# Kernel tuning notes

Measured on AMD Instinct MI355X. Metric: run time of the kernel, lower is better.

## Reference

```python
import jax, jax.numpy as jnp
import numpy as np


def _gcn(x, ei, W, b):
    """PyG-style GCNConv: add self-loops, symmetric deg^-1/2 normalization,
    linear transform, scatter-sum aggregation at target nodes, then bias."""
    n = x.shape[0]
    loops = jnp.arange(n)
    src = jnp.concatenate([ei[0], loops])  # message sources
    dst = jnp.concatenate([ei[1], loops])  # aggregation targets
    deg = jax.ops.segment_sum(jnp.ones(src.shape[0], x.dtype), dst, num_segments=n)
    dinv = jnp.where(deg > 0, jax.lax.rsqrt(deg), jnp.zeros_like(deg))
    h = x @ W  # [N, H]
    norm = (dinv[src] * dinv[dst])[:, None]
    out = jax.ops.segment_sum(h[src] * norm, dst, num_segments=n)
    return out + b


def setup_inputs() -> dict:
    N, E, C, H, O, HOPS = 50000, 1600000, 256, 256, 40, 3
    key = jax.random.key(0)
    ks = jax.random.split(key, 12)

    def xav(k, shp):
        # xavier_uniform with relu gain, as in init_weights
        fan_in, fan_out = shp[-2], shp[-1]
        lim = float(np.sqrt(2.0) * np.sqrt(6.0 / (fan_in + fan_out)))
        return jax.random.uniform(k, shp, jnp.float32, -lim, lim)

    return {
        "x": jax.random.normal(ks[0], (N, C), jnp.float32),
        "edge_index": jax.random.randint(ks[1], (2, E), 0, N),
        "new_edge_indexs": jax.random.randint(ks[2], (HOPS, 2, E), 0, N),
        "W_mlp": xav(ks[3], (C, H)),
        "b_mlp": jnp.zeros((H,), jnp.float32),
        "We1": xav(ks[4], (C, H)),
        "be1": jnp.zeros((H,), jnp.float32),
        "We2": xav(ks[5], (H, H)),
        "be2": jnp.zeros((H,), jnp.float32),
        "Wh": xav(ks[6], (HOPS, C, H)),
        "bh": jnp.zeros((HOPS, H), jnp.float32),
        "att": jnp.ones((HOPS + 2,), jnp.float32),
        "Wc": xav(ks[7], (H * (HOPS + 2), O)),
        "bc": jnp.zeros((O,), jnp.float32),
    }


def reference(x, edge_index, new_edge_indexs, W_mlp, b_mlp, We1, be1, We2, be2,
              Wh, bh, att, Wc, bc):
    hops = Wh.shape[0]
    mask = jax.nn.softmax(att)  # softmax over branch attention weights

    mlp = jax.nn.relu(x @ W_mlp + b_mlp) * mask[0]

    e = jax.nn.relu(_gcn(x, edge_index, We1, be1))
    # dropout(p=0.5) is identity in eval mode
    e = jax.nn.relu(_gcn(e, edge_index, We2, be2)) * mask[1]

    # NOTE: original code uses mask[i+1] per hop (hop 0 shares mask[1] with extra_conv)
    outs = [jax.nn.relu(_gcn(x, new_edge_indexs[i], Wh[i], bh[i])) * mask[i + 1]
            for i in range(hops)]

    z = jnp.concatenate(outs + [e, mlp], axis=1)  # [N, H*(hops+2)]
    z = z @ Wc + bc
    return jax.nn.log_softmax(z, axis=-1)
```

## Files before the change

### kernel.cpp

```cpp
#include <hip/hip_runtime.h>
#include <hip/hip_bf16.h>

typedef unsigned short u16;
typedef unsigned int u32;
typedef unsigned char u8;

typedef __bf16 bf16x8 __attribute__((ext_vector_type(8)));
typedef float f32x4 __attribute__((ext_vector_type(4)));

__device__ __forceinline__ u16 f2b(float f) {
    u32 u = __float_as_uint(f);
    u32 r = u + 0x7fffu + ((u >> 16) & 1u);
    return (u16)(r >> 16);
}
__device__ __forceinline__ u8 f2e4m3(float v) {
    return (u8)(__builtin_amdgcn_cvt_pk_fp8_f32(v, v, 0, false) & 0xff);
}
__device__ __forceinline__ void acc16(float* a, uint4 v) {
    u32 w[4] = {v.x, v.y, v.z, v.w};
#pragma unroll
    for (int q = 0; q < 4; ++q) {
        auto p0 = __builtin_amdgcn_cvt_pk_f32_fp8(w[q], false);
        auto p1 = __builtin_amdgcn_cvt_pk_f32_fp8(w[q], true);
        a[q * 4 + 0] += p0[0]; a[q * 4 + 1] += p0[1];
        a[q * 4 + 2] += p1[0]; a[q * 4 + 3] += p1[1];
    }
}

#define SA 72
#define BSHIFT 8
#define BMAX 256
#define BCAP 12288
#define BINCHUNK 4096
#define GEMM_SMEM (128 * SA * 2 * 2)

__global__ void pack_all(const float* __restrict__ x, u16* __restrict__ x16, int PB, int N,
                         const float* __restrict__ W_mlp, const float* __restrict__ We1,
                         const float* __restrict__ We2, const float* __restrict__ Wh,
                         u16* __restrict__ wt, int HOPS,
                         const float* __restrict__ Wc, u16* __restrict__ wct, int O, int NB, int WCB,
                         const float* __restrict__ att, float* __restrict__ mask,
                         int* __restrict__ bcnt, int SETS) {
    int b = blockIdx.x, t = threadIdx.x;
    if (b < PB) {
        long g = (long)b * 256 + t;
        if (g * 4 < (long)N * 256) {
            float4 v = reinterpret_cast<const float4*>(x)[g];
            ushort4 o; o.x = f2b(v.x); o.y = f2b(v.y); o.z = f2b(v.z); o.w = f2b(v.w);
            reinterpret_cast<ushort4*>(x16)[g] = o;
        }
        return;
    }
    b -= PB;
    int WB = (3 + HOPS) * 256;
    if (b < WB) {
        int y = b >> 8, ib = b & 255;
        const float* W = (y == 0) ? W_mlp : (y == 1) ? We1 : (y == 2) ? We2
                                          : (Wh + (size_t)(y - 3) * 65536);
        int idx = ib * 256 + t;
        int n = idx >> 8, k = idx & 255;
        wt[(size_t)y * 65536 + idx] = f2b(W[k * 256 + n]);
        return;
    }
    b -= WB;
    if (b < WCB) {
        int idx = b * 256 + t;
        if (idx < NB * 48 * 256) {
            int bb = idx / (48 * 256), r = idx - bb * 48 * 256;
            int n = r >> 8, k = r & 255;
            float v = (n < O) ? Wc[((size_t)(bb * 256 + k)) * O + n] : 0.f;
            wct[idx] = f2b(v);
        }
        return;
    }
    for (int i = t; i < SETS * BMAX; i += 256) bcnt[i] = 0;
    if (t == 0) {
        float m = -3.4e38f;
        for (int i = 0; i < NB; ++i) m = fmaxf(m, att[i]);
        float s = 0.f;
        for (int i = 0; i < NB; ++i) { float e = __expf(att[i] - m); mask[i] = e; s += e; }
        for (int i = 0; i < NB; ++i) mask[i] /= s;
    }
}


__global__ __launch_bounds__(256) void bin_edges(
    const int* __restrict__ ei, const int* __restrict__ nei, int E, int B,
    int* __restrict__ bcnt, u32* __restrict__ binned) {
    int set = blockIdx.y;
    const int* src = (set == 0) ? ei : (nei + (size_t)(set - 1) * 2 * E);
    const int* dst = src + E;
    __shared__ u32 ebuf[BINCHUNK];
    __shared__ int hist[BMAX], resv[BMAX], lbase[BMAX], lcur[BMAX], s[BMAX];
    int t = threadIdx.x;
    hist[t] = 0; lcur[t] = 0;
    __syncthreads();
    int base = blockIdx.x * BINCHUNK;
    int lim = min(base + BINCHUNK, E);
    for (int i = base + t; i < lim; i += 256)
        atomicAdd(&hist[dst[i] >> BSHIFT], 1);
    __syncthreads();
    int h = hist[t];
    if (t < B && h > 0) resv[t] = atomicAdd(&bcnt[set * BMAX + t], h);
    s[t] = h;
    __syncthreads();
    for (int off = 1; off < 256; off <<= 1) {
        int x = s[t];
        int add = (t >= off) ? s[t - off] : 0;
        __syncthreads();
        s[t] = x + add;
        __syncthreads();
    }
    lbase[t] = s[t] - h;
    __syncthreads();
    for (int i = base + t; i < lim; i += 256) {
        int d = dst[i];
        int b = d >> BSHIFT;
        int p = atomicAdd(&lcur[b], 1);
        ebuf[lbase[b] + p] = (u32)src[i] | ((u32)d << 16);
    }
    __syncthreads();
    int cnt = lim - base;
    for (int i = t; i < cnt; i += 256) {
        u32 pk = ebuf[i];
        int b = (int)(pk >> (16 + BSHIFT));
        int gpos = resv[b] + (i - lbase[b]);
        if (gpos < BCAP)
            binned[((size_t)set * BMAX + b) * BCAP + gpos] = pk;
    }
}

__global__ void bscan(const int* __restrict__ bcnt, int* __restrict__ bbase,
                      int* __restrict__ rp, int N, int E, int B) {
    int set = blockIdx.x, t = threadIdx.x;
    int v = (t < B) ? bcnt[set * BMAX + t] : 0;
    __shared__ int s[256];
    s[t] = v; __syncthreads();
    for (int off = 1; off < 256; off <<= 1) {
        int x = s[t];
        int add = (t >= off) ? s[t - off] : 0;
        __syncthreads();
        s[t] = x + add;
        __syncthreads();
    }
    bbase[set * BMAX + t] = s[t] - v;
    if (t == 0) rp[(size_t)set * (N + 1) + N] = E;
}

__global__ __launch_bounds__(256) void bucket_build(
    const u32* __restrict__ binned, const int* __restrict__ bcnt,
    const int* __restrict__ bbase, int* __restrict__ rp, float* __restrict__ dinv,
    u16* __restrict__ colAll, int E, int N) {
    int set = blockIdx.y;
    int b = blockIdx.x;
    int t = threadIdx.x;
    int nb = bcnt[set * BMAX + b];
    int base = bbase[set * BMAX + b];
    const u32* bin = binned + ((size_t)set * BMAX + b) * BCAP;
    __shared__ int s[256], lcur[256];
    s[t] = 0; lcur[t] = 0;
    __syncthreads();
    for (int i = t; i < nb; i += 256)
        atomicAdd(&s[(bin[i] >> 16) & 255], 1);
    __syncthreads();
    int deg = s[t];
    __syncthreads();
    for (int off = 1; off < 256; off <<= 1) {
        int x = s[t];
        int add = (t >= off) ? s[t - off] : 0;
        __syncthreads();
        s[t] = x + add;
        __syncthreads();
    }
    int ex = s[t] - deg;
    __syncthreads();
    s[t] = ex;
    int node = (b << BSHIFT) + t;
    if (node < N) {
        rp[(size_t)set * (N + 1) + node] = base + ex;
        dinv[(size_t)set * N + node] = rsqrtf((float)(deg + 1));
    }
    __syncthreads();
    for (int i = t; i < nb; i += 256) {
        u32 pk = bin[i];
        int dl = (int)((pk >> 16) & 255);
        int pos = base + s[dl] + atomicAdd(&lcur[dl], 1);
        colAll[(size_t)set * E + pos] = (u16)(pk & 0xffffu);
    }
}

__device__ __forceinline__ void gemm_body(char* smemraw, int bx, int by,
                                          const u16* __restrict__ A, const u16* __restrict__ Bt,
                                          void* __restrict__ outv, const float* bias,
                                          const float* dinv, int mode,
                                          const float* maskp, int M) {
    u16* lsA = (u16*)smemraw;
    u16* lsB = (u16*)(smemraw + 128 * SA * 2);
    const int tid = threadIdx.x;
    const int rowBase = bx * 128, colBase = by * 128;
    const int w = tid >> 6, l = tid & 63;
    const int wm = w >> 1, wn = w & 1;
    const int lrow = l & 15, lkg = l >> 4;
    f32x4 acc[4][4] = {};
    for (int kt = 0; kt < 4; ++kt) {
        const int k0 = kt * 64;
#pragma unroll
        for (int q = 0; q < 4; ++q) {
            int g = q * 256 + tid;
            int m = g >> 3, gq = g & 7;
            int grow = rowBase + m;
            int k = k0 + gq * 8;
            uint4 v = make_uint4(0, 0, 0, 0);
            if (grow < M) v = *reinterpret_cast<const uint4*>(A + (size_t)grow * 256 + k);
            *reinterpret_cast<uint4*>(&lsA[m * SA + gq * 8]) = v;
            uint4 vb = *reinterpret_cast<const uint4*>(Bt + (size_t)(colBase + m) * 256 + k);
            *reinterpret_cast<uint4*>(&lsB[m * SA + gq * 8]) = vb;
        }
        __syncthreads();
#pragma unroll
        for (int kk = 0; kk < 2; ++kk) {
            bf16x8 af[4], bfr[4];
            int kg8 = (kk * 4 + lkg) * 8;
#pragma unroll
            for (int mf = 0; mf < 4; ++mf)
                af[mf] = *reinterpret_cast<const bf16x8*>(&lsA[(wm * 64 + mf * 16 + lrow) * SA + kg8]);
#pragma unroll
            for (int nf = 0; nf < 4; ++nf)
                bfr[nf] = *reinterpret_cast<const bf16x8*>(&lsB[(wn * 64 + nf * 16 + lrow) * SA + kg8]);
#pragma unroll
            for (int mf = 0; mf < 4; ++mf)
#pragma unroll
                for (int nf = 0; nf < 4; ++nf)
                    acc[mf][nf] = __builtin_amdgcn_mfma_f32_16x16x32_bf16(af[mf], bfr[nf], acc[mf][nf], 0, 0, 0);
        }
        __syncthreads();
    }
    float mk = (mode == 0) ? maskp[0] : 1.f;
#pragma unroll
    for (int mf = 0; mf < 4; ++mf) {
#pragma unroll
        for (int r = 0; r < 4; ++r) {
            int row = rowBase + wm * 64 + mf * 16 + lkg * 4 + r;
            if (row >= M) continue;
            float dv = (mode == 1) ? dinv[row] : 0.f;
#pragma unroll
            for (int nf = 0; nf < 4; ++nf) {
                int colG = colBase + wn * 64 + nf * 16 + lrow;
                float v = acc[mf][nf][r];
                if (mode == 0) {
                    v = fmaxf(v + bias[colG], 0.f) * mk;
                    ((u16*)outv)[(size_t)row * 256 + colG] = f2b(v);
                } else {
                    ((u8*)outv)[(size_t)row * 256 + colG] = f2e4m3(v * dv);
                }
            }
        }
    }
}

__global__ __launch_bounds__(256) void gemm5(
    const u16* __restrict__ A, const u16* __restrict__ wt,
    u16* b_out, u8* f_h0, u8* f_h1, u8* f_h2, u8* f_e1,
    const float* __restrict__ b_mlp, const float* __restrict__ dinv,
    const float* __restrict__ maskp, int N, int GB) {
    __shared__ alignas(16) char smem[GEMM_SMEM];
    int bid = blockIdx.x;
    int c = bid & 7;
    int k = bid >> 3;
    int g = c + 8 * (k / 10);
    int m = k % 10;
    if (g >= GB) return;
    int br = m >> 1, half = m & 1;
    const u16* Bt; void* out; const float* dv = nullptr; int mode;
    if (br == 0)      { Bt = wt;              out = b_out; mode = 0; }
    else if (br == 1) { Bt = wt + 3 * 65536;  out = f_h0;  mode = 1; dv = dinv + (size_t)1 * N; }
    else if (br == 2) { Bt = wt + 4 * 65536;  out = f_h1;  mode = 1; dv = dinv + (size_t)2 * N; }
    else if (br == 3) { Bt = wt + 5 * 65536;  out = f_h2;  mode = 1; dv = dinv + (size_t)3 * N; }
    else              { Bt = wt + 1 * 65536;  out = f_e1;  mode = 1; dv = dinv; }
    gemm_body(smem, g, half, A, Bt, out, b_mlp, dv, mode, maskp, N);
}

__global__ __launch_bounds__(256) void gemm_k(const u16* __restrict__ A, const u16* __restrict__ Bt,
                                              u8* __restrict__ out, const float* __restrict__ dinv,
                                              int M) {
    __shared__ alignas(16) char smem[GEMM_SMEM];
    gemm_body(smem, blockIdx.x, blockIdx.y, A, Bt, out, nullptr, dinv, 1, nullptr, M);
}

__global__ __launch_bounds__(256) void agg_gcn(
    const u8* __restrict__ hp, const int* __restrict__ rp, const u16* __restrict__ colv,
    const float* __restrict__ dinv, const float* __restrict__ bias,
    const float* __restrict__ maskp, int maskIdx, u16* __restrict__ outb, int N) {
    int node = blockIdx.x * 4 + (threadIdx.x >> 6);
    if (node >= N) return;
    const int l = threadIdx.x & 63;
    const int slot = l >> 4, li = l & 15;
    const uint4* hv = reinterpret_cast<const uint4*>(hp);
    float a[16] = {0.f, 0.f, 0.f, 0.f, 0.f, 0.f, 0.f, 0.f,
                   0.f, 0.f, 0.f, 0.f, 0.f, 0.f, 0.f, 0.f};
    if (slot == 0) {
        uint4 v = hv[(size_t)node * 16 + li];
        acc16(a, v);
    }
    int beg = rp[node], end = rp[node + 1];
    int j = beg;
    for (; j + 16 <= end; j += 16) {
        int s0 = colv[j + slot];
        int s1 = colv[j + 4 + slot];
        int s2 = colv[j + 8 + slot];
        int s3 = colv[j + 12 + slot];
        uint4 v0 = hv[(size_t)s0 * 16 + li];
        uint4 v1 = hv[(size_t)s1 * 16 + li];
        uint4 v2 = hv[(size_t)s2 * 16 + li];
        uint4 v3 = hv[(size_t)s3 * 16 + li];
        acc16(a, v0); acc16(a, v1); acc16(a, v2); acc16(a, v3);
    }
    for (; j + 4 <= end; j += 4) {
        int s = colv[j + slot];
        acc16(a, hv[(size_t)s * 16 + li]);
    }
    if (j + slot < end) {
        int s = colv[j + slot];
        acc16(a, hv[(size_t)s * 16 + li]);
    }
#pragma unroll
    for (int q = 0; q < 16; ++q) {
        a[q] += __shfl_xor(a[q], 16);
        a[q] += __shfl_xor(a[q], 32);
    }
    if (slot == 0) {
        float dv = dinv[node];
        float mk = (maskIdx >= 0) ? maskp[maskIdx] : 1.f;
        int ch = li * 16;
        u32 o[8];
#pragma unroll
        for (int q = 0; q < 8; ++q) {
            float e0 = fmaxf(fmaf(a[2 * q + 0], dv, bias[ch + 2 * q + 0]), 0.f) * mk;
            float e1 = fmaxf(fmaf(a[2 * q + 1], dv, bias[ch + 2 * q + 1]), 0.f) * mk;
            o[q] = (u32)f2b(e0) | ((u32)f2b(e1) << 16);
        }
        uint4* ob = reinterpret_cast<uint4*>(outb) + (size_t)node * 32 + li * 2;
        ob[0] = make_uint4(o[0], o[1], o[2], o[3]);
        ob[1] = make_uint4(o[4], o[5], o[6], o[7]);
    }
}

template <int MODE>
__global__ __launch_bounds__(256) void logit_gemm(const u16* __restrict__ A,
                                                  const u16* __restrict__ Wct,
                                                  const float* __restrict__ bc,
                                                  float* __restrict__ out, int M) {
    int l = threadIdx.x & 63;
    int rowBase = blockIdx.x * 64 + (threadIdx.x >> 6) * 16;
    if (rowBase >= M) return;
    int lrow = l & 15, lkg = l >> 4;
    int ar = rowBase + lrow; if (ar >= M) ar = M - 1;
    f32x4 acc[3] = {};
#pragma unroll
    for (int kt = 0; kt < 8; ++kt) {
        bf16x8 a = *reinterpret_cast<const bf16x8*>(A + (size_t)ar * 256 + kt * 32 + lkg * 8);
#pragma unroll
        for (int nf = 0; nf < 3; ++nf) {
            bf16x8 b = *reinterpret_cast<const bf16x8*>(Wct + (size_t)(nf * 16 + lrow) * 256 + kt * 32 + lkg * 8);
            acc[nf] = __builtin_amdgcn_mfma_f32_16x16x32_bf16(a, b, acc[nf], 0, 0, 0);
        }
    }
    if (MODE != 2) {
#pragma unroll
        for (int nf = 0; nf < 3; ++nf) {
            int col = nf * 16 + lrow;
            if (col < 40) {
#pragma unroll
                for (int r = 0; r < 4; ++r) {
                    int row = rowBase + lkg * 4 + r;
                    if (row < M) {
                        if (MODE == 1) out[(size_t)row * 40 + col] = acc[nf][r] + bc[col];
                        else           out[(size_t)row * 40 + col] += acc[nf][r];
                    }
                }
            }
        }
    } else {
#pragma unroll
        for (int r = 0; r < 4; ++r) {
            int row = rowBase + lkg * 4 + r;
            float z[3];
#pragma unroll
            for (int nf = 0; nf < 3; ++nf) {
                int col = nf * 16 + lrow;
                z[nf] = -3.4e38f;
                if (col < 40 && row < M) z[nf] = out[(size_t)row * 40 + col] + acc[nf][r];
            }
            float m = fmaxf(fmaxf(z[0], z[1]), z[2]);
#pragma unroll
            for (int off = 1; off < 16; off <<= 1) m = fmaxf(m, __shfl_xor(m, off));
            float s = 0.f;
#pragma unroll
            for (int nf = 0; nf < 3; ++nf) s += (z[nf] > -1e38f) ? __expf(z[nf] - m) : 0.f;
#pragma unroll
            for (int off = 1; off < 16; off <<= 1) s += __shfl_xor(s, off);
            float lg = __logf(s);
#pragma unroll
            for (int nf = 0; nf < 3; ++nf) {
                int col = nf * 16 + lrow;
                if (col < 40 && row < M) out[(size_t)row * 40 + col] = z[nf] - m - lg;
            }
        }
    }
}


extern "C" void kernel_launch(void* const* d_in, const int* in_sizes, int n_in,
                              void* d_out, int out_size, void* d_ws, size_t ws_size,
                              hipStream_t stream) {
    (void)n_in; (void)out_size; (void)ws_size;
    const float* x     = (const float*)d_in[0];
    const int*   ei    = (const int*)d_in[1];
    const int*   nei   = (const int*)d_in[2];
    const float* W_mlp = (const float*)d_in[3];
    const float* b_mlp = (const float*)d_in[4];
    const float* We1   = (const float*)d_in[5];
    const float* be1   = (const float*)d_in[6];
    const float* We2   = (const float*)d_in[7];
    const float* be2   = (const float*)d_in[8];
    const float* Wh    = (const float*)d_in[9];
    const float* bh    = (const float*)d_in[10];
    const float* att   = (const float*)d_in[11];
    const float* Wc    = (const float*)d_in[12];
    const float* bc    = (const float*)d_in[13];
    float* out = (float*)d_out;

    const int N    = in_sizes[0] / 256;
    const int E    = in_sizes[1] / 2;
    const int HOPS = in_sizes[10] / 256;
    const int O    = in_sizes[13];
    const int SETS = HOPS + 1;
    const int NB   = HOPS + 2;
    const int B    = (N + 255) >> 8;

    char* p = (char*)d_ws;
    auto carve = [&](size_t bytes) { char* r = p; p += (bytes + 255) & ~(size_t)255; return r; };
    u16* x16 = (u16*)carve((size_t)N * 256 * 2);
    u16* b0  = (u16*)carve((size_t)N * 256 * 2);
    u16* b1  = (u16*)carve((size_t)N * 256 * 2);
    u8*  f0  = (u8*)carve((size_t)N * 256);
    u8*  f1  = (u8*)carve((size_t)N * 256);
    u8*  f2  = (u8*)carve((size_t)N * 256);
    u8*  f3  = (u8*)carve((size_t)N * 256);
    u8*  f4  = (u8*)carve((size_t)N * 256);
    u16* wt  = (u16*)carve((size_t)(3 + HOPS) * 65536 * 2);
    u16* wct = (u16*)carve((size_t)NB * 48 * 256 * 2);
    float* mask = (float*)carve(256);
    float* dinv = (float*)carve((size_t)SETS * N * 4);
    int* rp    = (int*)carve((size_t)SETS * (N + 1) * 4);
    int* bcnt  = (int*)carve((size_t)SETS * BMAX * 4);
    int* bbase = (int*)carve((size_t)SETS * BMAX * 4);
    u16* colAll = (u16*)carve((size_t)SETS * E * 2);
    u32* binned = (u32*)f0;

    const int PB  = (N * 64 + 255) / 256;
    const int WCB = (NB * 48 * 256 + 255) / 256;
    const int GB  = (N + 127) / 128;
    const int LB  = (N + 63) / 64;
    const int AB  = (N + 3) / 4;
    auto wct_b = [&](int b) { return wct + (size_t)b * 48 * 256; };

    {
        int grid = PB + (3 + HOPS) * 256 + WCB + 1;
        pack_all<<<grid, 256, 0, stream>>>(x, x16, PB, N, W_mlp, We1, We2, Wh, wt, HOPS,
                                           Wc, wct, O, NB, WCB, att, mask, bcnt, SETS);
    }
    {
        dim3 g((E + BINCHUNK - 1) / BINCHUNK, SETS);
        bin_edges<<<g, 256, 0, stream>>>(ei, nei, E, B, bcnt, binned);
    }
    bscan<<<SETS, 256, 0, stream>>>(bcnt, bbase, rp, N, E, B);
    {
        dim3 g(B, SETS);
        bucket_build<<<g, 256, 0, stream>>>(binned, bcnt, bbase, rp, dinv, colAll, E, N);
    }
    {
        int GBpad = ((GB + 7) / 8) * 8;
        gemm5<<<10 * GBpad, 256, 0, stream>>>(x16, wt, b0, f0, f1, f2, f3,
                                              b_mlp, dinv, mask, N, GB);
    }
    logit_gemm<1><<<LB, 256, 0, stream>>>(b0, wct_b(NB - 1), bc, out, N);
    agg_gcn<<<AB, 256, 0, stream>>>(f0, rp + (size_t)1 * (N + 1), colAll + (size_t)1 * E,
                                    dinv + (size_t)1 * N, bh + 0 * 256, mask, 1, b0, N);
    logit_gemm<0><<<LB, 256, 0, stream>>>(b0, wct_b(0), bc, out, N);
    agg_gcn<<<AB, 256, 0, stream>>>(f1, rp + (size_t)2 * (N + 1), colAll + (size_t)2 * E,
                                    dinv + (size_t)2 * N, bh + 1 * 256, mask, 2, b1, N);
    logit_gemm<0><<<LB, 256, 0, stream>>>(b1, wct_b(1), bc, out, N);
    agg_gcn<<<AB, 256, 0, stream>>>(f2, rp + (size_t)3 * (N + 1), colAll + (size_t)3 * E,
                                    dinv + (size_t)3 * N, bh + 2 * 256, mask, 3, b0, N);
    logit_gemm<0><<<LB, 256, 0, stream>>>(b0, wct_b(2), bc, out, N);
    agg_gcn<<<AB, 256, 0, stream>>>(f3, rp, colAll, dinv, be1, mask, -1, b1, N);
    gemm_k<<<dim3(GB, 2), 256, 0, stream>>>(b1, wt + 2 * 65536, f4, dinv, N);
    agg_gcn<<<AB, 256, 0, stream>>>(f4, rp, colAll, dinv, be2, mask, 1, b0, N);
    logit_gemm<2><<<LB, 256, 0, stream>>>(b0, wct_b(HOPS), bc, out, N);
}
```

Measured before the change: 659.4 us.

## Fuse edge binning into prep kernel and batch three hop aggregations and logits

Merges edge binning with the packing/weight-transposing prep kernel, replacing the in-kernel counter zeroing with a memset. The three hop GCN aggregations now run as one grid, and their logit contributions are computed in one kernel that accumulates all three branches before a single read-modify-write of the output. This reduces kernel launches and tail idle time and lets independent work overlap, at the cost of an extra bf16 buffer and larger combined grids.

Result: faster. 634.3 us (-3.8%).

```diff
diff --git a/kernel.cpp b/kernel.cpp
--- a/kernel.cpp
+++ b/kernel.cpp
@@ -34,14 +34,60 @@
 #define BINCHUNK 4096
 #define GEMM_SMEM (128 * SA * 2 * 2)
 
-__global__ void pack_all(const float* __restrict__ x, u16* __restrict__ x16, int PB, int N,
-                         const float* __restrict__ W_mlp, const float* __restrict__ We1,
-                         const float* __restrict__ We2, const float* __restrict__ Wh,
-                         u16* __restrict__ wt, int HOPS,
-                         const float* __restrict__ Wc, u16* __restrict__ wct, int O, int NB, int WCB,
-                         const float* __restrict__ att, float* __restrict__ mask,
-                         int* __restrict__ bcnt, int SETS) {
+__global__ __launch_bounds__(256) void prep(
+    const int* __restrict__ ei, const int* __restrict__ nei, int E, int B, int SETS,
+    int* __restrict__ bcnt, u32* __restrict__ binned, int binB,
+    const float* __restrict__ x, u16* __restrict__ x16, int PB, int N,
+    const float* __restrict__ W_mlp, const float* __restrict__ We1,
+    const float* __restrict__ We2, const float* __restrict__ Wh,
+    u16* __restrict__ wt, int HOPS,
+    const float* __restrict__ Wc, u16* __restrict__ wct, int O, int NB, int WCB,
+    const float* __restrict__ att, float* __restrict__ mask) {
+    __shared__ u32 ebuf[BINCHUNK];
+    __shared__ int hist[BMAX], resv[BMAX], lbase[BMAX], lcur[BMAX], s[BMAX];
     int b = blockIdx.x, t = threadIdx.x;
+    if (b < binB * SETS) {
+        int cx = b / SETS, set = b % SETS;
+        const int* src = (set == 0) ? ei : (nei + (size_t)(set - 1) * 2 * E);
+        const int* dst = src + E;
+        hist[t] = 0; lcur[t] = 0;
+        __syncthreads();
+        int base = cx * BINCHUNK;
+        int lim = min(base + BINCHUNK, E);
+        for (int i = base + t; i < lim; i += 256)
+            atomicAdd(&hist[dst[i] >> BSHIFT], 1);
+        __syncthreads();
+        int h = hist[t];
+        if (t < B && h > 0) resv[t] = atomicAdd(&bcnt[set * BMAX + t], h);
+        s[t] = h;
+        __syncthreads();
+        for (int off = 1; off < 256; off <<= 1) {
+            int x2 = s[t];
+            int add = (t >= off) ? s[t - off] : 0;
+            __syncthreads();
+            s[t] = x2 + add;
+            __syncthreads();
+        }
+        lbase[t] = s[t] - h;
+        __syncthreads();
+        for (int i = base + t; i < lim; i += 256) {
+            int d = dst[i];
+            int bb = d >> BSHIFT;
+            int p = atomicAdd(&lcur[bb], 1);
+            ebuf[lbase[bb] + p] = (u32)src[i] | ((u32)d << 16);
+        }
+        __syncthreads();
+        int cnt = lim - base;
+        for (int i = t; i < cnt; i += 256) {
+            u32 pk = ebuf[i];
+            int bb = (int)(pk >> (16 + BSHIFT));
+            int gpos = resv[bb] + (i - lbase[bb]);
+            if (gpos < BCAP)
+                binned[((size_t)set * BMAX + bb) * BCAP + gpos] = pk;
+        }
+        return;
+    }
+    b -= binB * SETS;
     if (b < PB) {
         long g = (long)b * 256 + t;
         if (g * 4 < (long)N * 256) {
@@ -73,60 +119,12 @@
         }
         return;
     }
-    for (int i = t; i < SETS * BMAX; i += 256) bcnt[i] = 0;
     if (t == 0) {
         float m = -3.4e38f;
         for (int i = 0; i < NB; ++i) m = fmaxf(m, att[i]);
-        float s = 0.f;
-        for (int i = 0; i < NB; ++i) { float e = __expf(att[i] - m); mask[i] = e; s += e; }
-        for (int i = 0; i < NB; ++i) mask[i] /= s;
-    }
-}
-
-
-__global__ __launch_bounds__(256) void bin_edges(
-    const int* __restrict__ ei, const int* __restrict__ nei, int E, int B,
-    int* __restrict__ bcnt, u32* __restrict__ binned) {
-    int set = blockIdx.y;
-    const int* src = (set == 0) ? ei : (nei + (size_t)(set - 1) * 2 * E);
-    const int* dst = src + E;
-    __shared__ u32 ebuf[BINCHUNK];
-    __shared__ int hist[BMAX], resv[BMAX], lbase[BMAX], lcur[BMAX], s[BMAX];
-    int t = threadIdx.x;
-    hist[t] = 0; lcur[t] = 0;
-    __syncthreads();
-    int base = blockIdx.x * BINCHUNK;
-    int lim = min(base + BINCHUNK, E);
-    for (int i = base + t; i < lim; i += 256)
-        atomicAdd(&hist[dst[i] >> BSHIFT], 1);
-    __syncthreads();
-    int h = hist[t];
-    if (t < B && h > 0) resv[t] = atomicAdd(&bcnt[set * BMAX + t], h);
-    s[t] = h;
-    __syncthreads();
-    for (int off = 1; off < 256; off <<= 1) {
-        int x = s[t];
-        int add = (t >= off) ? s[t - off] : 0;
-        __syncthreads();
-        s[t] = x + add;
-        __syncthreads();
-    }
-    lbase[t] = s[t] - h;
-    __syncthreads();
-    for (int i = base + t; i < lim; i += 256) {
-        int d = dst[i];
-        int b = d >> BSHIFT;
-        int p = atomicAdd(&lcur[b], 1);
-        ebuf[lbase[b] + p] = (u32)src[i] | ((u32)d << 16);
-    }
-    __syncthreads();
-    int cnt = lim - base;
-    for (int i = t; i < cnt; i += 256) {
-        u32 pk = ebuf[i];
-        int b = (int)(pk >> (16 + BSHIFT));
-        int gpos = resv[b] + (i - lbase[b]);
-        if (gpos < BCAP)
-            binned[((size_t)set * BMAX + b) * BCAP + gpos] = pk;
+        float s2 = 0.f;
+        for (int i = 0; i < NB; ++i) { float e = __expf(att[i] - m); mask[i] = e; s2 += e; }
+        for (int i = 0; i < NB; ++i) mask[i] /= s2;
     }
 }
 
@@ -287,11 +285,12 @@
     gemm_body(smem, blockIdx.x, blockIdx.y, A, Bt, out, nullptr, dinv, 1, nullptr, M);
 }
 
-__global__ __launch_bounds__(256) void agg_gcn(
-    const u8* __restrict__ hp, const int* __restrict__ rp, const u16* __restrict__ colv,
-    const float* __restrict__ dinv, const float* __restrict__ bias,
-    const float* __restrict__ maskp, int maskIdx, u16* __restrict__ outb, int N) {
-    int node = blockIdx.x * 4 + (threadIdx.x >> 6);
+__device__ __forceinline__ void agg_body(int blk, const u8* __restrict__ hp,
+                                         const int* __restrict__ rp, const u16* __restrict__ colv,
+                                         const float* __restrict__ dinv, const float* __restrict__ bias,
+                                         const float* __restrict__ maskp, int maskIdx,
+                                         u16* __restrict__ outb, int N) {
+    int node = blk * 4 + (threadIdx.x >> 6);
     if (node >= N) return;
     const int l = threadIdx.x & 63;
     const int slot = l >> 4, li = l & 15;
@@ -345,6 +344,27 @@
     }
 }
 
+__global__ __launch_bounds__(256) void agg_gcn(
+    const u8* __restrict__ hp, const int* __restrict__ rp, const u16* __restrict__ colv,
+    const float* __restrict__ dinv, const float* __restrict__ bias,
+    const float* __restrict__ maskp, int maskIdx, u16* __restrict__ outb, int N) {
+    agg_body(blockIdx.x, hp, rp, colv, dinv, bias, maskp, maskIdx, outb, N);
+}
+
+__global__ __launch_bounds__(256) void agg3(
+    const u8* f0, const u8* f1, const u8* f2,
+    const int* __restrict__ rp, const u16* __restrict__ colAll,
+    const float* __restrict__ dinv, const float* __restrict__ bh,
+    const float* __restrict__ maskp, u16* b0, u16* b1, u16* b2, int N, int E, int AB) {
+    int j = blockIdx.x / AB;
+    int blk = blockIdx.x - j * AB;
+    const u8* hp = (j == 0) ? f0 : (j == 1) ? f1 : f2;
+    u16* ob = (j == 0) ? b0 : (j == 1) ? b1 : b2;
+    int set = j + 1;
+    agg_body(blk, hp, rp + (size_t)set * (N + 1), colAll + (size_t)set * E,
+             dinv + (size_t)set * N, bh + (size_t)j * 256, maskp, j + 1, ob, N);
+}
+
 template <int MODE>
 __global__ __launch_bounds__(256) void logit_gemm(const u16* __restrict__ A,
                                                   const u16* __restrict__ Wct,
@@ -404,6 +424,42 @@
             for (int nf = 0; nf < 3; ++nf) {
                 int col = nf * 16 + lrow;
                 if (col < 40 && row < M) out[(size_t)row * 40 + col] = z[nf] - m - lg;
+            }
+        }
+    }
+}
+
+__global__ __launch_bounds__(256) void logit3(
+    const u16* __restrict__ A0, const u16* __restrict__ A1, const u16* __restrict__ A2,
+    const u16* __restrict__ wct, float* __restrict__ out, int M) {
+    int l = threadIdx.x & 63;
+    int rowBase = blockIdx.x * 64 + (threadIdx.x >> 6) * 16;
+    if (rowBase >= M) return;
+    int lrow = l & 15, lkg = l >> 4;
+    int ar = rowBase + lrow; if (ar >= M) ar = M - 1;
+    f32x4 acc[3] = {};
+#pragma unroll
+    for (int br = 0; br < 3; ++br) {
+        const u16* A = (br == 0) ? A0 : (br == 1) ? A1 : A2;
+        const u16* Wct = wct + (size_t)br * 48 * 256;
+#pragma unroll
+        for (int kt = 0; kt < 8; ++kt) {
+            bf16x8 a = *reinterpret_cast<const bf16x8*>(A + (size_t)ar * 256 + kt * 32 + lkg * 8);
+#pragma unroll
+            for (int nf = 0; nf < 3; ++nf) {
+                bf16x8 b = *reinterpret_cast<const bf16x8*>(Wct + (size_t)(nf * 16 + lrow) * 256 + kt * 32 + lkg * 8);
+                acc[nf] = __builtin_amdgcn_mfma_f32_16x16x32_bf16(a, b, acc[nf], 0, 0, 0);
+            }
+        }
+    }
+#pragma unroll
+    for (int nf = 0; nf < 3; ++nf) {
+        int col = nf * 16 + lrow;
+        if (col < 40) {
+#pragma unroll
+            for (int r = 0; r < 4; ++r) {
+                int row = rowBase + lkg * 4 + r;
+                if (row < M) out[(size_t)row * 40 + col] += acc[nf][r];
             }
         }
     }
@@ -443,6 +499,7 @@
     u16* x16 = (u16*)carve((size_t)N * 256 * 2);
     u16* b0  = (u16*)carve((size_t)N * 256 * 2);
     u16* b1  = (u16*)carve((size_t)N * 256 * 2);
+    u16* b2  = (u16*)carve((size_t)N * 256 * 2);
     u8*  f0  = (u8*)carve((size_t)N * 256);
     u8*  f1  = (u8*)carve((size_t)N * 256);
     u8*  f2  = (u8*)carve((size_t)N * 256);
@@ -458,21 +515,20 @@
     u16* colAll = (u16*)carve((size_t)SETS * E * 2);
     u32* binned = (u32*)f0;
 
-    const int PB  = (N * 64 + 255) / 256;
-    const int WCB = (NB * 48 * 256 + 255) / 256;
-    const int GB  = (N + 127) / 128;
-    const int LB  = (N + 63) / 64;
-    const int AB  = (N + 3) / 4;
+    const int PB   = (N * 64 + 255) / 256;
+    const int WCB  = (NB * 48 * 256 + 255) / 256;
+    const int GB   = (N + 127) / 128;
+    const int LB   = (N + 63) / 64;
+    const int AB   = (N + 3) / 4;
+    const int binB = (E + BINCHUNK - 1) / BINCHUNK;
     auto wct_b = [&](int b) { return wct + (size_t)b * 48 * 256; };
 
+    hipMemsetAsync(bcnt, 0, (size_t)SETS * BMAX * 4, stream);
     {
-        int grid = PB + (3 + HOPS) * 256 + WCB + 1;
-        pack_all<<<grid, 256, 0, stream>>>(x, x16, PB, N, W_mlp, We1, We2, Wh, wt, HOPS,
-                                           Wc, wct, O, NB, WCB, att, mask, bcnt, SETS);
-    }
-    {
-        dim3 g((E + BINCHUNK - 1) / BINCHUNK, SETS);
-        bin_edges<<<g, 256, 0, stream>>>(ei, nei, E, B, bcnt, binned);
+        int grid = binB * SETS + PB + (3 + HOPS) * 256 + WCB + 1;
+        prep<<<grid, 256, 0, stream>>>(ei, nei, E, B, SETS, bcnt, binned, binB,
+                                       x, x16, PB, N, W_mlp, We1, We2, Wh, wt, HOPS,
+                                       Wc, wct, O, NB, WCB, att, mask);
     }
     bscan<<<SETS, 256, 0, stream>>>(bcnt, bbase, rp, N, E, B);
     {
@@ -485,15 +541,9 @@
                                               b_mlp, dinv, mask, N, GB);
     }
     logit_gemm<1><<<LB, 256, 0, stream>>>(b0, wct_b(NB - 1), bc, out, N);
-    agg_gcn<<<AB, 256, 0, stream>>>(f0, rp + (size_t)1 * (N + 1), colAll + (size_t)1 * E,
-                                    dinv + (size_t)1 * N, bh + 0 * 256, mask, 1, b0, N);
-    logit_gemm<0><<<LB, 256, 0, stream>>>(b0, wct_b(0), bc, out, N);
-    agg_gcn<<<AB, 256, 0, stream>>>(f1, rp + (size_t)2 * (N + 1), colAll + (size_t)2 * E,
-                                    dinv + (size_t)2 * N, bh + 1 * 256, mask, 2, b1, N);
-    logit_gemm<0><<<LB, 256, 0, stream>>>(b1, wct_b(1), bc, out, N);
-    agg_gcn<<<AB, 256, 0, stream>>>(f2, rp + (size_t)3 * (N + 1), colAll + (size_t)3 * E,
-                                    dinv + (size_t)3 * N, bh + 2 * 256, mask, 3, b0, N);
-    logit_gemm<0><<<LB, 256, 0, stream>>>(b0, wct_b(2), bc, out, N);
+    agg3<<<3 * AB, 256, 0, stream>>>(f0, f1, f2, rp, colAll, dinv, bh, mask,
+                                     b0, b1, b2, N, E, AB);
+    logit3<<<LB, 256, 0, stream>>>(b0, b1, b2, wct, out, N);
     agg_gcn<<<AB, 256, 0, stream>>>(f3, rp, colAll, dinv, be1, mask, -1, b1, N);
     gemm_k<<<dim3(GB, 2), 256, 0, stream>>>(b1, wt + 2 * 65536, f4, dinv, N);
     agg_gcn<<<AB, 256, 0, stream>>>(f4, rp, colAll, dinv, be2, mask, 1, b0, N);
```
